# Kernel optimization log

Hardware: AMD Instinct MI355X
Metric: run time of the kernel (lower is better)

Reference implementation:

```python
import jax, jax.numpy as jnp
import numpy as np

B, N, DIN, H, D = 16, 1024, 128, 4, 32  # batch, n_agents, input_dim, heads, head_dim
NEG = -9e15


def setup_inputs() -> dict:
    key = jax.random.key(0)
    k1, k2, k3, k4 = jax.random.split(key, 4)
    x = jax.random.normal(k1, (B, N, DIN), jnp.float32)
    adj = jax.random.randint(k2, (B, N, N), 0, 2, jnp.int32)
    # params (xavier-ish scale)
    W = jax.random.normal(k3, (DIN, H * D), jnp.float32) * np.float32(1.0 / np.sqrt(DIN))
    b = jnp.zeros((H * D,), jnp.float32)
    a = jax.random.normal(k4, (2 * D, 1), jnp.float32) * np.float32(0.1)
    return {"x": x, "adj": adj, "W": W, "b": b, "a": a}


def reference(x, adj, W, b, a):
    Bb, Nn, _ = x.shape
    h = (x @ W + b).reshape(Bb, Nn, H, D)              # [B,N,H,D]
    # GAT trick: concat([h_i,h_j]) @ a == h_i@a[:D] + h_j@a[D:]
    a_i, a_j = a[:D, 0], a[D:, 0]
    e_i = jnp.einsum('bnhd,d->bnh', h, a_i)
    e_j = jnp.einsum('bnhd,d->bnh', h, a_j)
    e = e_i[:, :, None, :] + e_j[:, None, :, :]        # [B,N,N,H]
    e = jnp.where(e > 0, e, 0.2 * e)                   # LeakyReLU(0.2)
    e = jnp.where(adj[..., None] > 0, e, NEG)          # adjacency mask
    attn = jax.nn.softmax(e, axis=2)                   # softmax over neighbors j
    out = jnp.einsum('bijh,bjhd->bihd', attn, h)       # per-head aggregation
    return out.reshape(Bb, Nn, H * D)                  # concat heads
```

## Files before the change

kernel.cpp:

```cpp
#include <hip/hip_runtime.h>
#include <hip/hip_bf16.h>

#define Bdim 16
#define Ndim 1024
#define Hh   4
#define HDc  128
#define L2E  1.4426950408889634f

typedef float  float4v  __attribute__((ext_vector_type(4)));
typedef int    int4v    __attribute__((ext_vector_type(4)));
typedef short  short8   __attribute__((ext_vector_type(8)));
typedef unsigned short ushort4v __attribute__((ext_vector_type(4)));

__device__ __forceinline__ unsigned short bf16_rne(float f) {
    unsigned u = __float_as_uint(f);
    u = u + 0x7FFFu + ((u >> 16) & 1u);
    return (unsigned short)(u >> 16);
}

__device__ __forceinline__ void gl_lds16(const void* g, void* l) {
    __builtin_amdgcn_global_load_lds(
        (const __attribute__((address_space(1))) unsigned int*)g,
        (__attribute__((address_space(3))) unsigned int*)l, 16, 0, 0);
}

__global__ __launch_bounds__(256) void split_w_kernel(
    const float* __restrict__ W, const float* __restrict__ bias,
    const float* __restrict__ a,
    unsigned short* __restrict__ WTh, unsigned short* __restrict__ WTl,
    float* __restrict__ bias2)
{
    const int t = threadIdx.x, blk = blockIdx.x;
    if (blk < 16) {
        int r  = blk * 8 + (t >> 5);
        int k0 = (t & 31) * 4;
        #pragma unroll
        for (int j = 0; j < 4; ++j) {
            float f = W[(size_t)(k0 + j) * HDc + r];
            unsigned short hi = bf16_rne(f);
            WTh[r * 128 + k0 + j] = hi;
            WTl[r * 128 + k0 + j] = bf16_rne(f - __uint_as_float((unsigned)hi << 16));
        }
    } else {
        #pragma unroll
        for (int rep = 0; rep < 2; ++rep) {
            int task = t + rep * 256;
            int row = task >> 2, hh = task & 3;
            float si = 0.f, sj = 0.f;
            #pragma unroll
            for (int d4 = 0; d4 < 8; ++d4) {
                float4v wv = *(const float4v*)(W + (size_t)row * HDc + hh * 32 + d4 * 4);
                float4v av = *(const float4v*)(a + d4 * 4);
                float4v bv = *(const float4v*)(a + 32 + d4 * 4);
                #pragma unroll
                for (int kk = 0; kk < 4; ++kk) {
                    si = fmaf(wv[kk], av[kk], si);
                    sj = fmaf(wv[kk], bv[kk], sj);
                }
            }
            float vi = si * L2E, vj = sj * L2E;
            unsigned short hi = bf16_rne(vi);
            WTh[(128 + hh) * 128 + row] = hi;
            WTl[(128 + hh) * 128 + row] = bf16_rne(vi - __uint_as_float((unsigned)hi << 16));
            unsigned short hj = bf16_rne(vj);
            WTh[(132 + hh) * 128 + row] = hj;
            WTl[(132 + hh) * 128 + row] = bf16_rne(vj - __uint_as_float((unsigned)hj << 16));
        }
        #pragma unroll
        for (int rp = 0; rp < 4; ++rp) {
            int idx = t + rp * 256;
            WTh[136 * 128 + idx] = 0;
            WTl[136 * 128 + idx] = 0;
        }
        if (t < 128) {
            bias2[t] = bias[t];
        } else if (t < 136) {
            int z = t - 128;
            const float* av = (z < 4) ? a : a + 32;
            int hh = z & 3;
            float s = 0.f;
            for (int d = 0; d < 32; ++d) s = fmaf(bias[hh * 32 + d], av[d], s);
            bias2[128 + z] = s * L2E;
        } else if (t < 144) {
            bias2[t] = 0.f;
        }
    }
}

__global__ __launch_bounds__(256, 1) void proj_kernel(
    const float* __restrict__ x,
    const unsigned short* __restrict__ WTg_h, const unsigned short* __restrict__ WTg_l,
    const float* __restrict__ bias2,
    unsigned short* __restrict__ hTh, float* __restrict__ eiT, float* __restrict__ ejT)
{
    __shared__ __align__(16) unsigned char smem[106496];
    char* xls  = (char*)smem;
    char* wtls = (char*)smem + 32768;

    const int t = threadIdx.x, lane = t & 63, w = t >> 6;
    const int l16 = lane & 15, q = lane >> 4;
    const int nb = blockIdx.x * 64;
    const int b = nb >> 10, nloc = nb & 1023;

    {
        const char* gx = (const char*)(x + (size_t)nb * 128);
        int rh = lane >> 5, m = lane & 31;
        #pragma unroll
        for (int d = 0; d < 8; ++d) {
            int r = w * 16 + d * 2 + rh;
            int mg = m ^ (r & 7);
            gl_lds16(gx + (size_t)r * 512 + mg * 16, xls + (size_t)w * 8192 + d * 1024);
        }
    }
    {
        int rh = lane >> 4, m = lane & 15;
        #pragma unroll
        for (int d = 0; d < 18; ++d) {
            int n = w * 18 + d;
            if (n < 36) {
                int r = n * 4 + rh;
                gl_lds16((const char*)WTg_h + (size_t)r * 256 + (m ^ (r & 15)) * 16,
                         wtls + (size_t)n * 1024);
            } else {
                int r = (n - 36) * 4 + rh;
                gl_lds16((const char*)WTg_l + (size_t)r * 256 + (m ^ (r & 15)) * 16,
                         wtls + (size_t)n * 1024);
            }
        }
    }
    __syncthreads();

    float4v C[9];
    #pragma unroll
    for (int nt = 0; nt < 9; ++nt) C[nt] = (float4v){0.f, 0.f, 0.f, 0.f};

    #pragma unroll
    for (int ks = 0; ks < 4; ++ks) {
        short8 Ah, Al;
        {
            int r = w * 16 + l16;
            int c0 = (ks * 8 + q * 2) ^ (l16 & 7);
            int c1 = (ks * 8 + q * 2 + 1) ^ (l16 & 7);
            float4v x0 = *(const float4v*)(xls + (size_t)r * 512 + c0 * 16);
            float4v x1 = *(const float4v*)(xls + (size_t)r * 512 + c1 * 16);
            #pragma unroll
            for (int e = 0; e < 8; ++e) {
                float f = (e < 4) ? x0[e] : x1[e - 4];
                unsigned short hi = bf16_rne(f);
                Ah[e] = (short)hi;
                Al[e] = (short)bf16_rne(f - __uint_as_float((unsigned)hi << 16));
            }
        }
        #pragma unroll
        for (int nt = 0; nt < 9; ++nt) {
            const char* wb = wtls + (size_t)(nt * 16 + l16) * 256 + ((ks * 4 + q) ^ l16) * 16;
            short8 Bh = *(const short8*)wb;
            short8 Bl = *(const short8*)(wb + 36864);
            C[nt] = __builtin_amdgcn_mfma_f32_16x16x32_bf16(Ah, Bh, C[nt], 0, 0, 0);
            C[nt] = __builtin_amdgcn_mfma_f32_16x16x32_bf16(Ah, Bl, C[nt], 0, 0, 0);
            C[nt] = __builtin_amdgcn_mfma_f32_16x16x32_bf16(Al, Bh, C[nt], 0, 0, 0);
        }
    }

    {
        int node = nloc + w * 16 + q * 4;
        #pragma unroll
        for (int nt = 0; nt < 8; ++nt) {
            int col = nt * 16 + l16;
            float bv = bias2[col];
            ushort4v h4;
            #pragma unroll
            for (int r = 0; r < 4; ++r) h4[r] = bf16_rne(C[nt][r] + bv);
            *(ushort4v*)(hTh + (size_t)(b * HDc + col) * Ndim + node) = h4;
        }
        float bv = bias2[128 + l16];
        float4v v = {C[8][0] + bv, C[8][1] + bv, C[8][2] + bv, C[8][3] + bv};
        if (l16 < 4)
            *(float4v*)(eiT + (size_t)(b * Hh + l16) * Ndim + node) = v;
        else if (l16 < 8)
            *(float4v*)(ejT + (size_t)(b * Hh + (l16 - 4)) * Ndim + node) = v;
    }
}

__global__ __launch_bounds__(256, 4) void gat_kernel(
    const int* __restrict__ adj, const unsigned short* __restrict__ hTh,
    const float* __restrict__ eiT, const float* __restrict__ ejT,
    float* __restrict__ out)
{
    __shared__ __align__(16) unsigned char smem[36864];
    unsigned int* pkl = (unsigned int*)smem;
    float* ejlf = (float*)(smem + 2048);
    char* hts = (char*)smem + 4096;

    const int t = threadIdx.x, lane = t & 63, w = t >> 6;
    const int L = blockIdx.x;
    const int b = (L & 7) + 8 * ((L >> 3) & 1);
    const int ibase = (L >> 4) * 16;
    const int i = lane & 15, q = lane >> 4;

    {
        const int m = lane & 31, rh = lane >> 5;
        const int r0 = w * 4 + rh;
        const int r1 = w * 4 + 2 + rh;
        const int4v* s0 = (const int4v*)(adj + ((size_t)(b * Ndim + ibase + r0)) * Ndim + m * 32);
        const int4v* s1 = (const int4v*)(adj + ((size_t)(b * Ndim + ibase + r1)) * Ndim + m * 32);
        int4v va[8], vb[8];
        #pragma unroll
        for (int u = 0; u < 8; ++u) va[u] = __builtin_nontemporal_load(s0 + u);
        #pragma unroll
        for (int u = 0; u < 8; ++u) vb[u] = __builtin_nontemporal_load(s1 + u);
        unsigned wa = 0, wb_ = 0;
        #pragma unroll
        for (int u = 0; u < 8; ++u) {
            unsigned na  = (unsigned)(va[u][0] | (va[u][1] << 1) | (va[u][2] << 2) | (va[u][3] << 3));
            unsigned nb_ = (unsigned)(vb[u][0] | (vb[u][1] << 1) | (vb[u][2] << 2) | (vb[u][3] << 3));
            wa  |= na  << (4 * u);
            wb_ |= nb_ << (4 * u);
        }
        pkl[r0 * 32 + ((m + r0) & 31)] = wa;
        pkl[r1 * 32 + ((m + r1) & 31)] = wb_;
    }
    const float my_ei = eiT[(size_t)(b * Hh + w) * Ndim + ibase + i];

    const char* ghh = (const char*)(hTh + (size_t)(b * HDc + w * 32) * Ndim);
    const char* gej = (const char*)(ejT + (size_t)(b * Hh) * Ndim);
    const int drow = lane >> 4;
    const int p16  = lane & 15;
    const char* hrow0 = hts + (w * 32 + i) * 256;
    const char* hrow1 = hts + (w * 32 + 16 + i) * 256;
    const float* ejw = ejlf + w * 128;

    float4v C0 = {0.f, 0.f, 0.f, 0.f};
    float4v C1 = {0.f, 0.f, 0.f, 0.f};
    float den_a = 0.f, den_b = 0.f;
    __syncthreads();

    for (int ch = 0; ch < 8; ++ch) {
        if (ch) __syncthreads();
        #pragma unroll
        for (int u = 0; u < 8; ++u) {
            int d = u * 4 + drow;
            int c = p16 ^ (d & 15);
            gl_lds16(ghh + (size_t)d * 2048 + ch * 256 + c * 16,
                     hts + (w * 32 + u * 4) * 256);
        }
        if (w < 2) {
            int hh = w * 2 + (lane >> 5);
            gl_lds16(gej + (size_t)hh * 4096 + ch * 512 + (lane & 31) * 16,
                     (char*)ejlf + w * 1024);
        }
        __syncthreads();

        #pragma unroll
        for (int jtl = 0; jtl < 4; ++jtl) {
            const int jt = ch * 4 + jtl;
            const int pc = ((jtl * 4 + q) ^ i) * 16;
            short8 Bh0 = *(const short8*)(hrow0 + pc);
            short8 Bh1 = *(const short8*)(hrow1 + pc);
            float4v e0 = *(const float4v*)(ejw + jtl * 32 + q * 8);
            float4v e1 = *(const float4v*)(ejw + jtl * 32 + q * 8 + 4);
            unsigned bits = (pkl[i * 32 + ((jt + i) & 31)] >> (q * 8)) & 0xffu;

            float p[8];
            #pragma unroll
            for (int k = 0; k < 8; ++k) {
                float ev = (k < 4) ? e0[k] : e1[k - 4];
                float e = my_ei + ev;
                float sL = fmaxf(e, 0.2f * e);
                float pe = ((bits >> k) & 1u) ? __builtin_amdgcn_exp2f(sL) : 0.f;
                if (k & 1) den_b += pe; else den_a += pe;
                p[k] = pe;
            }
            union { __hip_bfloat162 h2[4]; short8 s8; } A;
            #pragma unroll
            for (int k2 = 0; k2 < 4; ++k2)
                A.h2[k2] = __float22bfloat162_rn(make_float2(p[2 * k2], p[2 * k2 + 1]));
            C0 = __builtin_amdgcn_mfma_f32_16x16x32_bf16(A.s8, Bh0, C0, 0, 0, 0);
            C1 = __builtin_amdgcn_mfma_f32_16x16x32_bf16(A.s8, Bh1, C1, 0, 0, 0);
        }
    }

    float den = den_a + den_b;
    den += __shfl_xor(den, 16);
    den += __shfl_xor(den, 32);

    float* outp = out + ((size_t)(b * Ndim + ibase)) * HDc + w * 32 + i;
    #pragma unroll
    for (int reg = 0; reg < 4; ++reg) {
        int row = q * 4 + reg;
        float rd = 1.0f / __shfl(den, row, 64);
        outp[(size_t)row * HDc]      = C0[reg] * rd;
        outp[(size_t)row * HDc + 16] = C1[reg] * rd;
    }
}

extern "C" void kernel_launch(void* const* d_in, const int* in_sizes, int n_in,
                              void* d_out, int out_size, void* d_ws, size_t ws_size,
                              hipStream_t stream) {
    const float* x    = (const float*)d_in[0];
    const int*   adj  = (const int*)d_in[1];
    const float* W    = (const float*)d_in[2];
    const float* bias = (const float*)d_in[3];
    const float* a    = (const float*)d_in[4];
    float* out = (float*)d_out;

    unsigned short* hTh = (unsigned short*)d_ws;
    float* eiT = (float*)(hTh + (size_t)Bdim * HDc * Ndim);
    float* ejT = eiT + (size_t)Bdim * Hh * Ndim;
    unsigned short* WTh = (unsigned short*)(ejT + (size_t)Bdim * Hh * Ndim);
    unsigned short* WTl = WTh + 144 * 128;
    float* bias2 = (float*)(WTl + 144 * 128);

    split_w_kernel<<<dim3(17), dim3(256), 0, stream>>>(W, bias, a, WTh, WTl, bias2);
    proj_kernel<<<dim3(256), dim3(256), 0, stream>>>(
        x, WTh, WTl, bias2, hTh, eiT, ejT);
    gat_kernel<<<dim3(1024), dim3(256), 0, stream>>>(
        adj, hTh, eiT, ejT, out);
}
```

Before: 166.3 us.

## Factor attention exponentials into per-node fp16 products and sum denominator via MFMA

Rewrites exp2(leakyrelu(ei+ej)) as max(2^ei*2^ej, 2^(0.2ei)*2^(0.2ej)), so per-node exponentials are computed once in the projection kernel and stored as fp16. The inner loop becomes packed fp16 multiplies, a max, and a mask taken from a small LDS lookup table, with no per-element exp. The softmax denominator comes from an extra MFMA against a ones vector instead of scalar adds and shuffles, and h and P switch from bf16 to fp16 MFMA. This risks fp16 overflow or underflow of the exponentials, since the inputs are not max-subtracted, and adds one MFMA per tile.

Measured after the change: 156.6 us. 1.06x faster.

```diff
diff --git a/kernel.cpp b/kernel.cpp
--- a/kernel.cpp
+++ b/kernel.cpp
@@ -11,17 +11,30 @@
 typedef int    int4v    __attribute__((ext_vector_type(4)));
 typedef short  short8   __attribute__((ext_vector_type(8)));
 typedef unsigned short ushort4v __attribute__((ext_vector_type(4)));
+typedef unsigned int   uint2v   __attribute__((ext_vector_type(2)));
+typedef _Float16 f16x2 __attribute__((ext_vector_type(2)));
+typedef _Float16 half8 __attribute__((ext_vector_type(8)));
 
 __device__ __forceinline__ unsigned short bf16_rne(float f) {
     unsigned u = __float_as_uint(f);
     u = u + 0x7FFFu + ((u >> 16) & 1u);
     return (unsigned short)(u >> 16);
 }
-
+__device__ __forceinline__ unsigned short f16u(float f) {
+    _Float16 h = (_Float16)f;
+    union { _Float16 h; unsigned short u; } c; c.h = h; return c.u;
+}
 __device__ __forceinline__ void gl_lds16(const void* g, void* l) {
     __builtin_amdgcn_global_load_lds(
         (const __attribute__((address_space(1))) unsigned int*)g,
         (__attribute__((address_space(3))) unsigned int*)l, 16, 0, 0);
+}
+__device__ __forceinline__ unsigned pmax_mask(unsigned EE, unsigned FF,
+                                              unsigned Ej, unsigned Fj, unsigned m) {
+    union { unsigned u; f16x2 h; } a, b, c, d, r;
+    a.u = EE; b.u = Ej; c.u = FF; d.u = Fj;
+    r.h = __builtin_elementwise_max(a.h * b.h, c.h * d.h);
+    return r.u & m;
 }
 
 __global__ __launch_bounds__(256) void split_w_kernel(
@@ -91,7 +104,9 @@
     const float* __restrict__ x,
     const unsigned short* __restrict__ WTg_h, const unsigned short* __restrict__ WTg_l,
     const float* __restrict__ bias2,
-    unsigned short* __restrict__ hTh, float* __restrict__ eiT, float* __restrict__ ejT)
+    unsigned short* __restrict__ hT,
+    unsigned short* __restrict__ eiE, unsigned short* __restrict__ eiF,
+    unsigned short* __restrict__ ejE, unsigned short* __restrict__ ejF)
 {
     __shared__ __align__(16) unsigned char smem[106496];
     char* xls  = (char*)smem;
@@ -170,27 +185,37 @@
             float bv = bias2[col];
             ushort4v h4;
             #pragma unroll
-            for (int r = 0; r < 4; ++r) h4[r] = bf16_rne(C[nt][r] + bv);
-            *(ushort4v*)(hTh + (size_t)(b * HDc + col) * Ndim + node) = h4;
+            for (int r = 0; r < 4; ++r) h4[r] = f16u(C[nt][r] + bv);
+            *(ushort4v*)(hT + (size_t)(b * HDc + col) * Ndim + node) = h4;
         }
         float bv = bias2[128 + l16];
-        float4v v = {C[8][0] + bv, C[8][1] + bv, C[8][2] + bv, C[8][3] + bv};
-        if (l16 < 4)
-            *(float4v*)(eiT + (size_t)(b * Hh + l16) * Ndim + node) = v;
-        else if (l16 < 8)
-            *(float4v*)(ejT + (size_t)(b * Hh + (l16 - 4)) * Ndim + node) = v;
+        if (l16 < 8) {
+            int hh = l16 & 3;
+            ushort4v Ev, Fv;
+            #pragma unroll
+            for (int r = 0; r < 4; ++r) {
+                float v = C[8][r] + bv;
+                Ev[r] = f16u(__builtin_amdgcn_exp2f(v));
+                Fv[r] = f16u(__builtin_amdgcn_exp2f(0.2f * v));
+            }
+            size_t off = (size_t)(b * Hh + hh) * Ndim + node;
+            if (l16 < 4) { *(ushort4v*)(eiE + off) = Ev; *(ushort4v*)(eiF + off) = Fv; }
+            else         { *(ushort4v*)(ejE + off) = Ev; *(ushort4v*)(ejF + off) = Fv; }
+        }
     }
 }
 
 __global__ __launch_bounds__(256, 4) void gat_kernel(
-    const int* __restrict__ adj, const unsigned short* __restrict__ hTh,
-    const float* __restrict__ eiT, const float* __restrict__ ejT,
+    const int* __restrict__ adj, const unsigned short* __restrict__ hT,
+    const unsigned short* __restrict__ eiE, const unsigned short* __restrict__ eiF,
+    const unsigned short* __restrict__ ejE, const unsigned short* __restrict__ ejF,
     float* __restrict__ out)
 {
-    __shared__ __align__(16) unsigned char smem[36864];
+    __shared__ __align__(16) unsigned char smem[40960];
     unsigned int* pkl = (unsigned int*)smem;
-    float* ejlf = (float*)(smem + 2048);
-    char* hts = (char*)smem + 4096;
+    unsigned int* lut = (unsigned int*)(smem + 2048);
+    char* ejl = (char*)smem + 4096;
+    char* hts = (char*)smem + 8192;
 
     const int t = threadIdx.x, lane = t & 63, w = t >> 6;
     const int L = blockIdx.x;
@@ -220,20 +245,36 @@
         pkl[r0 * 32 + ((m + r0) & 31)] = wa;
         pkl[r1 * 32 + ((m + r1) & 31)] = wb_;
     }
-    const float my_ei = eiT[(size_t)(b * Hh + w) * Ndim + ibase + i];
-
-    const char* ghh = (const char*)(hTh + (size_t)(b * HDc + w * 32) * Ndim);
-    const char* gej = (const char*)(ejT + (size_t)(b * Hh) * Ndim);
+    if (t < 16) {
+        lut[t * 2]     = ((t & 1) ? 0xFFFFu : 0u) | ((t & 2) ? 0xFFFF0000u : 0u);
+        lut[t * 2 + 1] = ((t & 4) ? 0xFFFFu : 0u) | ((t & 8) ? 0xFFFF0000u : 0u);
+    }
+    const size_t eidx = (size_t)(b * Hh + w) * Ndim + ibase + i;
+    const unsigned Eu = eiE[eidx], Fu = eiF[eidx];
+    const unsigned EE = Eu | (Eu << 16);
+    const unsigned FF = Fu | (Fu << 16);
+    __syncthreads();
+
+    const char* ghh = (const char*)(hT + (size_t)(b * HDc + w * 32) * Ndim);
     const int drow = lane >> 4;
     const int p16  = lane & 15;
+    const char* gE = (const char*)(ejE + (size_t)(b * Hh + w) * Ndim);
+    const char* gF = (const char*)(ejF + (size_t)(b * Hh + w) * Ndim);
+    const int l5 = lane & 31;
+    const char* esrc = (l5 < 16) ? gE + l5 * 16 : gF + (l5 - 16) * 16;
+
     const char* hrow0 = hts + (w * 32 + i) * 256;
-    const char* hrow1 = hts + (w * 32 + 16 + i) * 256;
-    const float* ejw = ejlf + w * 128;
+    const char* hrow1 = hrow0 + 16 * 256;
+    const char* ejw   = ejl + w * 1024;
+    const uint2v* lut2 = (const uint2v*)lut;
+
+    half8 ONES;
+    #pragma unroll
+    for (int e = 0; e < 8; ++e) ONES[e] = (_Float16)1.0f;
 
     float4v C0 = {0.f, 0.f, 0.f, 0.f};
     float4v C1 = {0.f, 0.f, 0.f, 0.f};
-    float den_a = 0.f, den_b = 0.f;
-    __syncthreads();
+    float4v C2 = {0.f, 0.f, 0.f, 0.f};
 
     for (int ch = 0; ch < 8; ++ch) {
         if (ch) __syncthreads();
@@ -244,51 +285,38 @@
             gl_lds16(ghh + (size_t)d * 2048 + ch * 256 + c * 16,
                      hts + (w * 32 + u * 4) * 256);
         }
-        if (w < 2) {
-            int hh = w * 2 + (lane >> 5);
-            gl_lds16(gej + (size_t)hh * 4096 + ch * 512 + (lane & 31) * 16,
-                     (char*)ejlf + w * 1024);
-        }
+        gl_lds16(esrc + ch * 256, ejl + w * 1024);
         __syncthreads();
 
         #pragma unroll
         for (int jtl = 0; jtl < 4; ++jtl) {
             const int jt = ch * 4 + jtl;
-            const int pc = ((jtl * 4 + q) ^ i) * 16;
-            short8 Bh0 = *(const short8*)(hrow0 + pc);
-            short8 Bh1 = *(const short8*)(hrow1 + pc);
-            float4v e0 = *(const float4v*)(ejw + jtl * 32 + q * 8);
-            float4v e1 = *(const float4v*)(ejw + jtl * 32 + q * 8 + 4);
+            const int sb = jtl * 4 + q;
+            half8 Bh0 = *(const half8*)(hrow0 + ((sb ^ i) << 4));
+            half8 Bh1 = *(const half8*)(hrow1 + ((sb ^ i) << 4));
+            int4v Ejp = *(const int4v*)(ejw + (sb << 4));
+            int4v Fjp = *(const int4v*)(ejw + 256 + (sb << 4));
             unsigned bits = (pkl[i * 32 + ((jt + i) & 31)] >> (q * 8)) & 0xffu;
-
-            float p[8];
-            #pragma unroll
-            for (int k = 0; k < 8; ++k) {
-                float ev = (k < 4) ? e0[k] : e1[k - 4];
-                float e = my_ei + ev;
-                float sL = fmaxf(e, 0.2f * e);
-                float pe = ((bits >> k) & 1u) ? __builtin_amdgcn_exp2f(sL) : 0.f;
-                if (k & 1) den_b += pe; else den_a += pe;
-                p[k] = pe;
-            }
-            union { __hip_bfloat162 h2[4]; short8 s8; } A;
-            #pragma unroll
-            for (int k2 = 0; k2 < 4; ++k2)
-                A.h2[k2] = __float22bfloat162_rn(make_float2(p[2 * k2], p[2 * k2 + 1]));
-            C0 = __builtin_amdgcn_mfma_f32_16x16x32_bf16(A.s8, Bh0, C0, 0, 0, 0);
-            C1 = __builtin_amdgcn_mfma_f32_16x16x32_bf16(A.s8, Bh1, C1, 0, 0, 0);
-        }
-    }
-
-    float den = den_a + den_b;
-    den += __shfl_xor(den, 16);
-    den += __shfl_xor(den, 32);
+            uint2v m0 = lut2[bits & 15];
+            uint2v m1 = lut2[bits >> 4];
+
+            union { unsigned u[4]; half8 v; } A;
+            A.u[0] = pmax_mask(EE, FF, (unsigned)Ejp[0], (unsigned)Fjp[0], m0[0]);
+            A.u[1] = pmax_mask(EE, FF, (unsigned)Ejp[1], (unsigned)Fjp[1], m0[1]);
+            A.u[2] = pmax_mask(EE, FF, (unsigned)Ejp[2], (unsigned)Fjp[2], m1[0]);
+            A.u[3] = pmax_mask(EE, FF, (unsigned)Ejp[3], (unsigned)Fjp[3], m1[1]);
+
+            C0 = __builtin_amdgcn_mfma_f32_16x16x32_f16(A.v, Bh0, C0, 0, 0, 0);
+            C1 = __builtin_amdgcn_mfma_f32_16x16x32_f16(A.v, Bh1, C1, 0, 0, 0);
+            C2 = __builtin_amdgcn_mfma_f32_16x16x32_f16(A.v, ONES, C2, 0, 0, 0);
+        }
+    }
 
     float* outp = out + ((size_t)(b * Ndim + ibase)) * HDc + w * 32 + i;
     #pragma unroll
     for (int reg = 0; reg < 4; ++reg) {
         int row = q * 4 + reg;
-        float rd = 1.0f / __shfl(den, row, 64);
+        float rd = 1.0f / C2[reg];
         outp[(size_t)row * HDc]      = C0[reg] * rd;
         outp[(size_t)row * HDc + 16] = C1[reg] * rd;
     }
@@ -304,16 +332,18 @@
     const float* a    = (const float*)d_in[4];
     float* out = (float*)d_out;
 
-    unsigned short* hTh = (unsigned short*)d_ws;
-    float* eiT = (float*)(hTh + (size_t)Bdim * HDc * Ndim);
-    float* ejT = eiT + (size_t)Bdim * Hh * Ndim;
-    unsigned short* WTh = (unsigned short*)(ejT + (size_t)Bdim * Hh * Ndim);
+    unsigned short* hT  = (unsigned short*)d_ws;
+    unsigned short* eiE = hT  + (size_t)Bdim * HDc * Ndim;
+    unsigned short* eiF = eiE + (size_t)Bdim * Hh * Ndim;
+    unsigned short* ejE = eiF + (size_t)Bdim * Hh * Ndim;
+    unsigned short* ejF = ejE + (size_t)Bdim * Hh * Ndim;
+    unsigned short* WTh = ejF + (size_t)Bdim * Hh * Ndim;
     unsigned short* WTl = WTh + 144 * 128;
     float* bias2 = (float*)(WTl + 144 * 128);
 
     split_w_kernel<<<dim3(17), dim3(256), 0, stream>>>(W, bias, a, WTh, WTl, bias2);
     proj_kernel<<<dim3(256), dim3(256), 0, stream>>>(
-        x, WTh, WTl, bias2, hTh, eiT, ejT);
+        x, WTh, WTl, bias2, hT, eiE, eiF, ejE, ejF);
     gat_kernel<<<dim3(1024), dim3(256), 0, stream>>>(
-        adj, hTh, eiT, ejT, out);
-}
+        adj, hT, eiE, eiF, ejE, ejF, out);
+}
```
